# Kernel tuning notes

Hardware: AMD Instinct MI355X
Metric: run time of the kernel (lower is better)

Reference implementation:

```python
import jax, jax.numpy as jnp
import numpy as np

TEMPERATURE = 0.2
NUMBER_CLASSES = 1000
LOSS_SCALE = 0.001

N, F = 8192, 256
M = 20000
DEPTH = 4


def setup_inputs() -> dict:
    key = jax.random.key(0)
    k1, k2, k3, k4 = jax.random.split(key, 4)
    gt_labels = jax.random.randint(k1, (N,), 0, NUMBER_CLASSES, dtype=jnp.int32)
    box_features = jax.random.normal(k2, (N, F), dtype=jnp.float32)
    memory = jax.random.normal(k3, (M, F), dtype=jnp.float32)
    trace_idx = jax.random.randint(k4, (NUMBER_CLASSES, DEPTH), 0, M, dtype=jnp.int32)
    return {"gt_labels": gt_labels, "box_features": box_features,
            "memory": memory, "trace_idx": trace_idx}


def reference(gt_labels, box_features, memory, trace_idx):
    # logits[i, j] = dot(f_i, m_j) / T  (the nested python loops fused into one GEMM)
    logits = jnp.einsum('nf,mf->nm', box_features, memory) / TEMPERATURE  # [N, M]
    # fenmu = sum_j exp(logits)  ->  log(fenmu) = logsumexp
    lse = jax.nn.logsumexp(logits, axis=-1)  # [N]
    # gather the trace entries for each item's label: [N, DEPTH]
    traces = trace_idx[gt_labels]  # [N, DEPTH]
    sel = jnp.take_along_axis(logits, traces, axis=1)  # [N, DEPTH]
    depth_w = jnp.arange(DEPTH, dtype=logits.dtype)  # gj = depth
    sum_gj = depth_w.sum()  # sum of layer weights (0+1+2+3)
    # per item: -sum_d gj * log(sim_d / fenmu) / sum_gj
    per_item = -jnp.sum((sel - lse[:, None]) * depth_w, axis=-1) / sum_gj  # [N]
    # background filter: items with label == number_classes contribute nothing
    fg = (gt_labels != NUMBER_CLASSES)
    loss = jnp.sum(jnp.where(fg, per_item, 0.0)) * LOSS_SCALE
    return loss
```

## Files before the change

kernel.cpp:

```cpp
#include <hip/hip_runtime.h>
#include <hip/hip_bf16.h>
#include <stdint.h>

#define NROWS 8192
#define FDIM 256
#define MCOLS 20000
#define NT32 625
#define MSPLIT 16
#define NCLS 1000
#define LOG2E 1.44269504088896f
#define LN2   0.69314718055994f


typedef short short8 __attribute__((ext_vector_type(8)));
typedef float f32x16 __attribute__((ext_vector_type(16)));

typedef __attribute__((address_space(3))) unsigned int lds_u32;
typedef const __attribute__((address_space(1))) unsigned int glb_u32;

__device__ __forceinline__ float ex2(float x) {
    float r;
    asm("v_exp_f32 %0, %1" : "=v"(r) : "v"(x));
    return r;
}

__device__ __forceinline__ unsigned short f2bf(float x) {
    unsigned u = __float_as_uint(x);
    unsigned r = (u + 0x7FFFu + ((u >> 16) & 1u)) >> 16;
    return (unsigned short)r;
}

__device__ __forceinline__ float vmax16(f32x16 v) {
    float x0 = fmaxf(fmaxf(v[0],  v[1]),  v[2]);
    float x1 = fmaxf(fmaxf(v[3],  v[4]),  v[5]);
    float x2 = fmaxf(fmaxf(v[6],  v[7]),  v[8]);
    float x3 = fmaxf(fmaxf(v[9],  v[10]), v[11]);
    float x4 = fmaxf(fmaxf(v[12], v[13]), v[14]);
    float x5 = fmaxf(fmaxf(x0, x1), x2);
    float x6 = fmaxf(fmaxf(x3, x4), v[15]);
    return fmaxf(x5, x6);
}

__global__ void conv_kernel(const float* __restrict__ in, unsigned short* __restrict__ out,
                            int n4, float scale) {
    int idx = blockIdx.x * blockDim.x + threadIdx.x;
    if (idx >= n4) return;
    float4 v = ((const float4*)in)[idx];
    ushort4 o;
    o.x = f2bf(v.x * scale); o.y = f2bf(v.y * scale);
    o.z = f2bf(v.z * scale); o.w = f2bf(v.w * scale);
    ((ushort4*)out)[idx] = o;
}

__global__ void sel_kernel(const int* __restrict__ gt, const float* __restrict__ F,
                           const float* __restrict__ Mem, const int* __restrict__ trace,
                           float* __restrict__ wsel) {
    int lane = threadIdx.x & 63, wid = threadIdx.x >> 6;
    int i = blockIdx.x * 4 + wid;
    int label = gt[i];
    float w = 0.0f;
    if (label >= 0 && label < NCLS) {
        float4 fv = ((const float4*)(F + (size_t)i * FDIM))[lane];
        #pragma unroll
        for (int d = 1; d <= 3; ++d) {
            int tr = trace[label * 4 + d];
            float4 mv = ((const float4*)(Mem + (size_t)tr * FDIM))[lane];
            float dot = fv.x*mv.x + fv.y*mv.y + fv.z*mv.z + fv.w*mv.w;
            #pragma unroll
            for (int off = 32; off >= 1; off >>= 1) dot += __shfl_xor(dot, off, 64);
            w += (float)d * dot;
        }
    }
    if (lane == 0) wsel[i] = w * 5.0f;
}

__global__ __launch_bounds__(256, 2) void lse_gemm(
        const unsigned short* __restrict__ Fb, const unsigned short* __restrict__ Mb,
        float* __restrict__ pm, float* __restrict__ ps) {
    __shared__ __align__(16) char smem[2 * 16384];

    const int split  = blockIdx.x;
    const int rowblk = blockIdx.y;
    const int tid  = threadIdx.x;
    const int lane = tid & 63, wid = tid >> 6;
    const int r0 = lane & 31;
    const int hi = lane >> 5;
    const int rowbase = rowblk * 256 + wid * 64;

    short8 al[16], ah[16];
    #pragma unroll
    for (int kk = 0; kk < 16; ++kk) {
        al[kk] = *(const short8*)(Fb + (size_t)(rowbase + r0)      * FDIM + kk * 16 + hi * 8);
        ah[kk] = *(const short8*)(Fb + (size_t)(rowbase + 32 + r0) * FDIM + kk * 16 + hi * 8);
    }
    #pragma unroll
    for (int kk = 0; kk < 16; ++kk) {
        asm volatile("" : "+v"(al[kk]));
        asm volatile("" : "+a"(ah[kk]));
    }

    float m0 = -3.0e38f, s0 = 0.0f, m1 = -3.0e38f, s1 = 0.0f;

    const int t0 = (split * NT32) / MSPLIT;
    const int t1 = ((split + 1) * NT32) / MSPLIT;

    int srcoff[4];
    #pragma unroll
    for (int c = 0; c < 4; ++c) {
        const int g = (wid * 4 + c) * 64 + lane;
        const int j = g >> 5, o = g & 31;
        srcoff[c] = j * 512 + ((o ^ j) << 4);
    }

#define STAGE(BUF, t)                                                              \
    do {                                                                           \
        const char* srcT = (const char*)Mb + (size_t)(t) * 16384;                  \
        _Pragma("unroll")                                                          \
        for (int c = 0; c < 4; ++c) {                                              \
            __builtin_amdgcn_global_load_lds(                                      \
                (glb_u32*)(srcT + srcoff[c]),                                      \
                (lds_u32*)(smem + (BUF) * 16384 + (wid * 4 + c) * 1024),           \
                16, 0, 0);                                                         \
        }                                                                          \
    } while (0)

    int roff[16];
    #pragma unroll
    for (int kk = 0; kk < 16; ++kk)
        roff[kk] = r0 * 512 + ((((kk << 1) | hi) ^ r0) << 4);

#define BODYC(BUF)                                                                 \
    do {                                                                           \
        f32x16 acc0 = {0,0,0,0,0,0,0,0,0,0,0,0,0,0,0,0};                           \
        f32x16 acc1 = {0,0,0,0,0,0,0,0,0,0,0,0,0,0,0,0};                           \
        __builtin_amdgcn_s_setprio(1);                                             \
        _Pragma("unroll")                                                          \
        for (int kk = 0; kk < 16; ++kk) {                                          \
            short8 b = *(const short8*)(smem + (BUF) * 16384 + roff[kk]);          \
            acc0 = __builtin_amdgcn_mfma_f32_32x32x16_bf16(b, al[kk], acc0, 0, 0, 0); \
            acc1 = __builtin_amdgcn_mfma_f32_32x32x16_bf16(b, ah[kk], acc1, 0, 0, 0); \
        }                                                                          \
        __builtin_amdgcn_s_setprio(0);                                             \
        {                                                                          \
            float nm = fmaxf(vmax16(acc0), m0);                                    \
            float p0 = 0.f, p1 = 0.f, p2 = 0.f, p3 = 0.f;                          \
            _Pragma("unroll")                                                      \
            for (int i = 0; i < 16; i += 4) {                                      \
                p0 += ex2(acc0[i]     - nm); p1 += ex2(acc0[i + 1] - nm);          \
                p2 += ex2(acc0[i + 2] - nm); p3 += ex2(acc0[i + 3] - nm);          \
            }                                                                      \
            s0 = fmaf(s0, ex2(m0 - nm), (p0 + p1) + (p2 + p3));                    \
            m0 = nm;                                                               \
        }                                                                          \
        {                                                                          \
            float nm = fmaxf(vmax16(acc1), m1);                                    \
            float p0 = 0.f, p1 = 0.f, p2 = 0.f, p3 = 0.f;                          \
            _Pragma("unroll")                                                      \
            for (int i = 0; i < 16; i += 4) {                                      \
                p0 += ex2(acc1[i]     - nm); p1 += ex2(acc1[i + 1] - nm);          \
                p2 += ex2(acc1[i + 2] - nm); p3 += ex2(acc1[i + 3] - nm);          \
            }                                                                      \
            s1 = fmaf(s1, ex2(m1 - nm), (p0 + p1) + (p2 + p3));                    \
            m1 = nm;                                                               \
        }                                                                          \
    } while (0)

    STAGE(0, t0);
    __syncthreads();

    int t = t0;
    while (t + 2 <= t1) {
        STAGE(1, t + 1);
        BODYC(0);
        __syncthreads();
        if (t + 2 < t1) STAGE(0, t + 2);
        BODYC(1);
        __syncthreads();
        t += 2;
    }
    if (t < t1) BODYC(0);

#undef BODYC
#undef STAGE

    {
        float om = __shfl_xor(m0, 32, 64);
        float os = __shfl_xor(s0, 32, 64);
        float nm = fmaxf(m0, om);
        float sf = fmaf(s0, ex2(m0 - nm), os * ex2(om - nm));
        if (lane < 32) {
            pm[split * NROWS + rowbase + lane] = nm;
            ps[split * NROWS + rowbase + lane] = sf;
        }
    }
    {
        float om = __shfl_xor(m1, 32, 64);
        float os = __shfl_xor(s1, 32, 64);
        float nm = fmaxf(m1, om);
        float sf = fmaf(s1, ex2(m1 - nm), os * ex2(om - nm));
        if (lane < 32) {
            pm[split * NROWS + rowbase + 32 + lane] = nm;
            ps[split * NROWS + rowbase + 32 + lane] = sf;
        }
    }
}

__global__ void finalize_kernel(const int* __restrict__ gt, const float* __restrict__ wsel,
                                const float* __restrict__ pm, const float* __restrict__ ps,
                                float* __restrict__ bpart) {
    int tid = threadIdx.x;
    int i = blockIdx.x * 256 + tid;
    float mv[MSPLIT];
    float M = -3.0e38f;
    #pragma unroll
    for (int k = 0; k < MSPLIT; ++k) { mv[k] = pm[k * NROWS + i]; M = fmaxf(M, mv[k]); }
    float S = 0.0f;
    #pragma unroll
    for (int k = 0; k < MSPLIT; ++k) S += ps[k * NROWS + i] * ex2(mv[k] - M);
    float lse = (M + __log2f(S)) * LN2;
    int label = gt[i];
    float per = (label >= 0 && label < NCLS) ? (lse - wsel[i] * (1.0f / 6.0f)) : 0.0f;
    #pragma unroll
    for (int off = 32; off >= 1; off >>= 1) per += __shfl_xor(per, off, 64);
    __shared__ float red[4];
    int lane = tid & 63, wid = tid >> 6;
    if (lane == 0) red[wid] = per;
    __syncthreads();
    if (tid == 0) bpart[blockIdx.x] = red[0] + red[1] + red[2] + red[3];
}

__global__ void sum_kernel(const float* __restrict__ bpart, float* __restrict__ out) {
    int tid = threadIdx.x;
    float v = (tid < 32) ? bpart[tid] : 0.0f;
    #pragma unroll
    for (int off = 32; off >= 1; off >>= 1) v += __shfl_xor(v, off, 64);
    if (tid == 0) out[0] = 0.001f * v;
}

extern "C" void kernel_launch(void* const* d_in, const int* in_sizes, int n_in,
                              void* d_out, int out_size, void* d_ws, size_t ws_size,
                              hipStream_t stream) {
    const int*   gt    = (const int*)d_in[0];
    const float* F     = (const float*)d_in[1];
    const float* Mem   = (const float*)d_in[2];
    const int*   trace = (const int*)d_in[3];
    float* out = (float*)d_out;

    char* w = (char*)d_ws;
    unsigned short* Mb = (unsigned short*)w;
    unsigned short* Fb = (unsigned short*)(w + 10240000);
    float* wsel  = (float*)(w + 14434304);
    float* pm    = (float*)(w + 14467072);
    float* ps    = (float*)(w + 14991360);
    float* bpart = (float*)(w + 15515648);

    conv_kernel<<<dim3((MCOLS * FDIM / 4) / 256), dim3(256), 0, stream>>>(Mem, Mb, MCOLS * FDIM / 4, 1.0f);
    conv_kernel<<<dim3((NROWS * FDIM / 4) / 256), dim3(256), 0, stream>>>(F, Fb, NROWS * FDIM / 4, 5.0f * LOG2E);
    sel_kernel<<<dim3(NROWS / 4), dim3(256), 0, stream>>>(gt, F, Mem, trace, wsel);
    lse_gemm<<<dim3(MSPLIT, NROWS / 256), dim3(256), 0, stream>>>(Fb, Mb, pm, ps);
    finalize_kernel<<<dim3(NROWS / 256), dim3(256), 0, stream>>>(gt, wsel, pm, ps, bpart);
    sum_kernel<<<dim3(1), dim3(64), 0, stream>>>(bpart, out);
}
```

Baseline: 118.3 us.

## Pre-swizzle memory bank into MFMA fragment order to simplify LDS staging

The bf16 conversion of the memory bank now writes each 32-column tile in the exact per-lane MFMA operand order. The GEMM can then stage tiles with a plain contiguous global_load_lds and read B fragments at lane*16 + kk*1024, with no XOR swizzle offset arrays. This removes the srcoff/roff index registers and gives conflict-free sequential LDS reads. It also drops the asm constraints that pinned half the A fragments to AGPRs, leaving register allocation to the compiler, which could change spilling or occupancy.

Measured after the change: 102.4 us. -13.5%, faster.

```diff
diff --git a/kernel.cpp b/kernel.cpp
--- a/kernel.cpp
+++ b/kernel.cpp
@@ -50,6 +50,20 @@
     o.x = f2bf(v.x * scale); o.y = f2bf(v.y * scale);
     o.z = f2bf(v.z * scale); o.w = f2bf(v.w * scale);
     ((ushort4*)out)[idx] = o;
+}
+
+__global__ void conv_mb2(const float* __restrict__ in, unsigned short* __restrict__ out) {
+    int g = blockIdx.x * 256 + threadIdx.x;
+    int s = g & 63, kk = (g >> 6) & 15, t = g >> 10;
+    const float* src = in + (size_t)(t * 32 + (s & 31)) * FDIM + kk * 16 + (s >> 5) * 8;
+    float4 v0 = ((const float4*)src)[0];
+    float4 v1 = ((const float4*)src)[1];
+    short8 w;
+    w[0] = (short)f2bf(v0.x); w[1] = (short)f2bf(v0.y);
+    w[2] = (short)f2bf(v0.z); w[3] = (short)f2bf(v0.w);
+    w[4] = (short)f2bf(v1.x); w[5] = (short)f2bf(v1.y);
+    w[6] = (short)f2bf(v1.z); w[7] = (short)f2bf(v1.w);
+    *(short8*)(out + (size_t)g * 8) = w;
 }
 
 __global__ void sel_kernel(const int* __restrict__ gt, const float* __restrict__ F,
@@ -75,7 +89,7 @@
 }
 
 __global__ __launch_bounds__(256, 2) void lse_gemm(
-        const unsigned short* __restrict__ Fb, const unsigned short* __restrict__ Mb,
+        const unsigned short* __restrict__ Fb, const unsigned short* __restrict__ Mb2,
         float* __restrict__ pm, float* __restrict__ ps) {
     __shared__ __align__(16) char smem[2 * 16384];
 
@@ -86,6 +100,7 @@
     const int r0 = lane & 31;
     const int hi = lane >> 5;
     const int rowbase = rowblk * 256 + wid * 64;
+    const int l16 = lane << 4;
 
     short8 al[16], ah[16];
     #pragma unroll
@@ -93,72 +108,55 @@
         al[kk] = *(const short8*)(Fb + (size_t)(rowbase + r0)      * FDIM + kk * 16 + hi * 8);
         ah[kk] = *(const short8*)(Fb + (size_t)(rowbase + 32 + r0) * FDIM + kk * 16 + hi * 8);
     }
-    #pragma unroll
-    for (int kk = 0; kk < 16; ++kk) {
-        asm volatile("" : "+v"(al[kk]));
-        asm volatile("" : "+a"(ah[kk]));
-    }
 
     float m0 = -3.0e38f, s0 = 0.0f, m1 = -3.0e38f, s1 = 0.0f;
 
     const int t0 = (split * NT32) / MSPLIT;
     const int t1 = ((split + 1) * NT32) / MSPLIT;
 
-    int srcoff[4];
-    #pragma unroll
-    for (int c = 0; c < 4; ++c) {
-        const int g = (wid * 4 + c) * 64 + lane;
-        const int j = g >> 5, o = g & 31;
-        srcoff[c] = j * 512 + ((o ^ j) << 4);
-    }
-
 #define STAGE(BUF, t)                                                              \
     do {                                                                           \
-        const char* srcT = (const char*)Mb + (size_t)(t) * 16384;                  \
+        const char* srcT = (const char*)Mb2 + (size_t)(t) * 16384 + l16;           \
         _Pragma("unroll")                                                          \
         for (int c = 0; c < 4; ++c) {                                              \
             __builtin_amdgcn_global_load_lds(                                      \
-                (glb_u32*)(srcT + srcoff[c]),                                      \
+                (glb_u32*)(srcT + (wid * 4 + c) * 1024),                           \
                 (lds_u32*)(smem + (BUF) * 16384 + (wid * 4 + c) * 1024),           \
                 16, 0, 0);                                                         \
         }                                                                          \
     } while (0)
 
-    int roff[16];
-    #pragma unroll
-    for (int kk = 0; kk < 16; ++kk)
-        roff[kk] = r0 * 512 + ((((kk << 1) | hi) ^ r0) << 4);
-
 #define BODYC(BUF)                                                                 \
     do {                                                                           \
-        f32x16 acc0 = {0,0,0,0,0,0,0,0,0,0,0,0,0,0,0,0};                           \
-        f32x16 acc1 = {0,0,0,0,0,0,0,0,0,0,0,0,0,0,0,0};                           \
+        const char* bp = smem + (BUF) * 16384 + l16;                               \
+        f32x16 accL = {0,0,0,0,0,0,0,0,0,0,0,0,0,0,0,0};                           \
+        f32x16 accH = {0,0,0,0,0,0,0,0,0,0,0,0,0,0,0,0};                           \
         __builtin_amdgcn_s_setprio(1);                                             \
         _Pragma("unroll")                                                          \
         for (int kk = 0; kk < 16; ++kk) {                                          \
-            short8 b = *(const short8*)(smem + (BUF) * 16384 + roff[kk]);          \
-            acc0 = __builtin_amdgcn_mfma_f32_32x32x16_bf16(b, al[kk], acc0, 0, 0, 0); \
-            acc1 = __builtin_amdgcn_mfma_f32_32x32x16_bf16(b, ah[kk], acc1, 0, 0, 0); \
+            short8 b = *(const short8*)(bp + kk * 1024);                           \
+            accL = __builtin_amdgcn_mfma_f32_32x32x16_bf16(b, al[kk], accL, 0, 0, 0); \
+            accH = __builtin_amdgcn_mfma_f32_32x32x16_bf16(b, ah[kk], accH, 0, 0, 0); \
         }                                                                          \
         __builtin_amdgcn_s_setprio(0);                                             \
         {                                                                          \
-            float nm = fmaxf(vmax16(acc0), m0);                                    \
+            float nm = fmaxf(vmax16(accL), m0);                                    \
             float p0 = 0.f, p1 = 0.f, p2 = 0.f, p3 = 0.f;                          \
             _Pragma("unroll")                                                      \
             for (int i = 0; i < 16; i += 4) {                                      \
-                p0 += ex2(acc0[i]     - nm); p1 += ex2(acc0[i + 1] - nm);          \
-                p2 += ex2(acc0[i + 2] - nm); p3 += ex2(acc0[i + 3] - nm);          \
+                p0 += ex2(accL[i]     - nm); p1 += ex2(accL[i + 1] - nm);          \
+                p2 += ex2(accL[i + 2] - nm); p3 += ex2(accL[i + 3] - nm);          \
             }                                                                      \
             s0 = fmaf(s0, ex2(m0 - nm), (p0 + p1) + (p2 + p3));                    \
             m0 = nm;                                                               \
         }                                                                          \
         {                                                                          \
-            float nm = fmaxf(vmax16(acc1), m1);                                    \
+            float nm = fmaxf(vmax16(accH), m1);                                    \
             float p0 = 0.f, p1 = 0.f, p2 = 0.f, p3 = 0.f;                          \
             _Pragma("unroll")                                                      \
             for (int i = 0; i < 16; i += 4) {                                      \
-                p0 += ex2(acc1[i]     - nm); p1 += ex2(acc1[i + 1] - nm);          \
-                p2 += ex2(acc1[i + 2] - nm); p3 += ex2(acc1[i + 3] - nm);          \
+                p0 += ex2(accH[i]     - nm); p1 += ex2(accH[i + 1] - nm);          \
+                p2 += ex2(accH[i + 2] - nm); p3 += ex2(accH[i + 3] - nm);          \
             }                                                                      \
             s1 = fmaf(s1, ex2(m1 - nm), (p0 + p1) + (p2 + p3));                    \
             m1 = nm;                                                               \
@@ -247,17 +245,17 @@
     float* out = (float*)d_out;
 
     char* w = (char*)d_ws;
-    unsigned short* Mb = (unsigned short*)w;
-    unsigned short* Fb = (unsigned short*)(w + 10240000);
+    unsigned short* Mb2 = (unsigned short*)w;
+    unsigned short* Fb  = (unsigned short*)(w + 10240000);
     float* wsel  = (float*)(w + 14434304);
     float* pm    = (float*)(w + 14467072);
     float* ps    = (float*)(w + 14991360);
     float* bpart = (float*)(w + 15515648);
 
-    conv_kernel<<<dim3((MCOLS * FDIM / 4) / 256), dim3(256), 0, stream>>>(Mem, Mb, MCOLS * FDIM / 4, 1.0f);
+    conv_mb2<<<dim3(2500), dim3(256), 0, stream>>>(Mem, Mb2);
     conv_kernel<<<dim3((NROWS * FDIM / 4) / 256), dim3(256), 0, stream>>>(F, Fb, NROWS * FDIM / 4, 5.0f * LOG2E);
     sel_kernel<<<dim3(NROWS / 4), dim3(256), 0, stream>>>(gt, F, Mem, trace, wsel);
-    lse_gemm<<<dim3(MSPLIT, NROWS / 256), dim3(256), 0, stream>>>(Fb, Mb, pm, ps);
+    lse_gemm<<<dim3(MSPLIT, NROWS / 256), dim3(256), 0, stream>>>(Fb, Mb2, pm, ps);
     finalize_kernel<<<dim3(NROWS / 256), dim3(256), 0, stream>>>(gt, wsel, pm, ps, bpart);
     sum_kernel<<<dim3(1), dim3(64), 0, stream>>>(bpart, out);
 }
```
